# Performance work log

Hardware: AMD Instinct MI355X
Metric: run time of the kernel (lower is better)

The kernel has to match this reference:

```python
import jax, jax.numpy as jnp
import numpy as np
from jax import lax

PRE_NMS_THRESH = 0.05
PRE_NMS_TOP_N = 1000
FINAL_NMS_THRESH = 0.4  # hardcoded in forward(): boxlist_nms(..., 0.4)
MIN_SIZE = 0
STRIDE = 4.0
NEG = -1e9

N, C, H, W = 32, 1, 384, 384


def setup_inputs() -> dict:
    key = jax.random.key(0)
    k1, k2 = jax.random.split(key)
    box_cls = jax.random.uniform(k1, (N, C, H, W), dtype=jnp.float32)
    box_regression = jax.random.normal(k2, (N, 4, H, W), dtype=jnp.float32) * 20.0
    image_sizes = jnp.full((N, 2), H * int(STRIDE), dtype=jnp.int32)
    return {"box_cls": box_cls, "box_regression": box_regression, "image_sizes": image_sizes}


def decode_boxes(quad):
    # quad: [N, 4, H, W]; EAST geometry decode at stride 4 -> xyxy
    n, _, h, w = quad.shape
    x = (jnp.arange(w, dtype=quad.dtype) * STRIDE)[None, :]   # [1, W]
    y = (jnp.arange(h, dtype=quad.dtype) * STRIDE)[:, None]   # [H, 1]
    ymin = y - quad[:, 0]
    xmax = x + quad[:, 1]
    ymax = y + quad[:, 2]
    xmin = x - quad[:, 3]
    return jnp.stack([xmin, ymin, xmax, ymax], axis=1)  # [N, 4, H, W] (permute (3,0,1,2))


def iou_matrix(b):
    # b: [K, 4] xyxy
    x1, y1, x2, y2 = b[:, 0], b[:, 1], b[:, 2], b[:, 3]
    area = jnp.clip(x2 - x1, 0) * jnp.clip(y2 - y1, 0)
    ix1 = jnp.maximum(x1[:, None], x1[None, :])
    iy1 = jnp.maximum(y1[:, None], y1[None, :])
    ix2 = jnp.minimum(x2[:, None], x2[None, :])
    iy2 = jnp.minimum(y2[:, None], y2[None, :])
    inter = jnp.clip(ix2 - ix1, 0) * jnp.clip(iy2 - iy1, 0)
    union = area[:, None] + area[None, :] - inter
    return inter / jnp.maximum(union, 1e-9)


def greedy_nms(boxes, init_keep):
    # boxes: [K, 4] sorted by descending score; init_keep: [K] bool
    K = boxes.shape[0]
    iou = iou_matrix(boxes)
    idx = jnp.arange(K)

    def body(i, keep):
        suppress = (iou[i] > FINAL_NMS_THRESH) & (idx > i)
        return jnp.where(keep[i], keep & ~suppress, keep)

    return lax.fori_loop(0, K, body, init_keep)


def _forward(box_cls, box_regression):
    n, c, h, w = box_cls.shape
    boxes = decode_boxes(box_regression)                       # [N, 4, H, W]
    boxes = boxes.transpose(0, 2, 3, 1).reshape(n, h * w, 4)   # [N, HW, 4]
    scores = box_cls.transpose(0, 2, 3, 1).reshape(n, h * w)   # [N, HW] (C=1)

    # threshold + conditional top-k (padding with NEG emulates variable counts)
    masked = jnp.where(scores > PRE_NMS_THRESH, scores, NEG)
    scores_k, idx_k = lax.top_k(masked, PRE_NMS_TOP_N)         # [N, K], sorted desc
    boxes_k = jnp.take_along_axis(boxes, idx_k[..., None], axis=1)  # [N, K, 4]

    valid = scores_k > PRE_NMS_THRESH
    ws = boxes_k[..., 2] - boxes_k[..., 0]
    hs = boxes_k[..., 3] - boxes_k[..., 1]
    valid = valid & (ws >= MIN_SIZE) & (hs >= MIN_SIZE)        # remove_small_boxes

    keep = jax.vmap(greedy_nms)(boxes_k, valid)                # [N, K]
    out = jnp.concatenate([boxes_k, scores_k[..., None]], axis=-1)
    out = out * keep[..., None].astype(out.dtype)              # [N, K, 5]
    return out, keep


def reference(box_cls, box_regression, image_sizes):
    return _forward(box_cls, box_regression)
```

## Files before the change

### kernel.cpp

```cpp
#include <hip/hip_runtime.h>
#include <stdint.h>

#define NIMG 32
#define WID 384
#define HW 147456
#define TOPK 1000
#define KPAD 1024
#define NBINS 512
#define BIN_SCALEF 512.0f
#define SEGCAP 128
#define CANDCAP 2048
#define THRESH 0.05f
#define PREF_C 0.99f
#define NMS_T 0.4f
#define NBLK 18
#define FINEBINS 256

typedef unsigned long long u64;
typedef unsigned int u32;

#define PCNT_OFF 0
#define PCAND_OFF 4096
#define PBOX_OFF  593920

__device__ __forceinline__ float area_of(float x0, float y0, float x1, float y1) {
  float a = fmaxf(x1 - x0, 0.0f) * fmaxf(y1 - y0, 0.0f);
  asm volatile("" : "+v"(a));
  return a;
}

__device__ __forceinline__ bool iou_gt(float ax0, float ay0, float ax1, float ay1, float aa,
                                       float bx0, float by0, float bx1, float by1, float ba) {
  float ix1 = fmaxf(ax0, bx0);
  float iy1 = fmaxf(ay0, by0);
  float ix2 = fminf(ax1, bx1);
  float iy2 = fminf(ay1, by1);
  float iw = fmaxf(ix2 - ix1, 0.0f);
  float ih = fmaxf(iy2 - iy1, 0.0f);
  float inter = iw * ih;
  asm volatile("" : "+v"(inter));
  float uni = fmaxf(aa + ba - inter, 1e-9f);
  return (inter / uni) > NMS_T;
}

__device__ __forceinline__ u64 shflxor64(u64 v, int m) {
  int lo = __shfl_xor((int)(u32)v, m, 64);
  int hi = __shfl_xor((int)(u32)(v >> 32), m, 64);
  return ((u64)(u32)hi << 32) | (u32)lo;
}

__device__ __forceinline__ u64 make_key(float s, u32 idx) {
  u32 ord = __float_as_uint(s) | 0x80000000u;
  return ((u64)ord << 32) | (u32)(~idx);
}

__device__ __forceinline__ float score_of(u64 key) {
  return __uint_as_float((u32)(key >> 32) & 0x7FFFFFFFu);
}

__device__ __forceinline__ int bin_of(float s) {
  int b = (int)(s * BIN_SCALEF);
  return b < 0 ? 0 : (b > NBINS - 1 ? NBINS - 1 : b);
}

__device__ __forceinline__ int finebin(u64 key) {
  float s = score_of(key);
  int b = (int)((s - 0.99f) * 25600.0f);
  return b < 0 ? 0 : (b > FINEBINS - 1 ? FINEBINS - 1 : b);
}

__global__ __launch_bounds__(256) void scan_kernel(const float* __restrict__ cls,
                                                   const float* __restrict__ reg,
                                                   u32* __restrict__ pcnt,
                                                   u64* __restrict__ pcand,
                                                   float4* __restrict__ pbox) {
  __shared__ u64 lbuf[SEGCAP];
  __shared__ u32 lcnt;
  const int n = blockIdx.y;
  const int tid = threadIdx.x;
  const int lane = tid & 63;
  if (tid == 0) lcnt = 0;
  __syncthreads();

  const float4* src = (const float4*)(cls + (size_t)n * HW) + blockIdx.x * 2048;
  float4 A[8];
#pragma unroll
  for (int v = 0; v < 8; v++) A[v] = src[tid + v * 256];

  const u64 ltmask = (1ull << lane) - 1ull;
#pragma unroll
  for (int v = 0; v < 8; v++) {
    float ss[4] = {A[v].x, A[v].y, A[v].z, A[v].w};
#pragma unroll
    for (int c = 0; c < 4; c++) {
      float s = ss[c];
      bool pc = s > PREF_C;
      u64 m = __ballot(pc);
      if (m) {
        int ldr = __ffsll(m) - 1;
        u32 wb = 0;
        if (lane == ldr) wb = atomicAdd(&lcnt, (u32)__popcll(m));
        wb = (u32)__shfl((int)wb, ldr, 64);
        if (pc) {
          u32 pos = wb + (u32)__popcll(m & ltmask);
          if (pos < SEGCAP) lbuf[pos] = make_key(s, (u32)((blockIdx.x * 2048 + tid + v * 256) * 4 + c));
        }
      }
    }
  }
  __syncthreads();
  const int seg = n * NBLK + blockIdx.x;
  if (tid == 0) pcnt[seg] = (lcnt > SEGCAP) ? 0xFFFFFFFFu : lcnt;
  u32 c = lcnt < SEGCAP ? lcnt : (u32)SEGCAP;
  const float* rb = reg + (size_t)n * 4 * HW;
  u64* pk = pcand + (size_t)seg * SEGCAP;
  float4* pb = pbox + (size_t)seg * SEGCAP;
  for (u32 i = tid; i < c; i += 256) {
    u64 key = lbuf[i];
    u32 idx = ~(u32)(key & 0xFFFFFFFFull);
    int iy = (int)idx / WID;
    int ix = (int)idx - iy * WID;
    float xx = (float)ix * 4.0f;
    float yy = (float)iy * 4.0f;
    float r0 = rb[idx];
    float r1 = rb[HW + idx];
    float r2 = rb[2 * HW + idx];
    float r3 = rb[3 * HW + idx];
    float4 box;
    box.y = yy - r0; box.z = xx + r1; box.w = yy + r2; box.x = xx - r3;
    pk[i] = key;
    pb[i] = box;
  }
}

#define REGCHAIN(K, JSTART) do {                                            \
    const bool desc_ = ((tid & ((K) >> 1)) == 0);                           \
    for (int j_ = (JSTART); j_ >= 2; j_ >>= 1) {                            \
      int h_ = j_ >> 1;                                                     \
      bool low_ = (tid & h_) == 0;                                          \
      u64 p0_ = shflxor64(e0, h_), p1_ = shflxor64(e1, h_);                 \
      bool tm_ = (low_ == desc_);                                           \
      e0 = tm_ ? (e0 > p0_ ? e0 : p0_) : (e0 < p0_ ? e0 : p0_);             \
      e1 = tm_ ? (e1 > p1_ ? e1 : p1_) : (e1 < p1_ ? e1 : p1_);             \
    }                                                                       \
    { u64 lo_ = e0 < e1 ? e0 : e1, hi_ = e0 < e1 ? e1 : e0;                 \
      e0 = desc_ ? hi_ : lo_; e1 = desc_ ? lo_ : hi_; }                     \
  } while (0)

__global__ __launch_bounds__(1024) void fused_kernel(const float* __restrict__ cls,
                                                     const float* __restrict__ reg,
                                                     const u32* __restrict__ pcnt,
                                                     const u64* __restrict__ pcand,
                                                     const float4* __restrict__ pbox,
                                                     float* __restrict__ out) {
  __shared__ __align__(16) unsigned char smem[90112];
  u64*    CKEY   = (u64*)smem;
  float4* CBOX   = (float4*)(smem + 16384);
  u32*    BINNED = (u32*)(smem + 49152);
  u64*    RKEY   = (u64*)(smem + 57344);
  float4* RBOX   = (float4*)(smem + 65536);
  float* vx    = (float*)smem;
  float* vy    = (float*)(smem + 4096);
  float* vz    = (float*)(smem + 8192);
  float* vw    = (float*)(smem + 12288);
  float* varea = (float*)(smem + 16384);
  u64*   mlds  = (u64*)(smem + 20480);

  __shared__ u32 BINSTART[FINEBINS + 1];
  __shared__ u32 HIST[FINEBINS];
  __shared__ u32 scnt[NBLK];
  __shared__ u32 soff[NBLK];
  __shared__ u32 bs[NBINS];
  __shared__ u32 stmp[64];
  __shared__ int stbin;
  __shared__ u32 sflag, sfc;
  __shared__ int sC;
  __shared__ u32 wcnt[16], woff[16];
  __shared__ int pc[136], pk[136];
  __shared__ int sV, snch, snp;
  __shared__ u64 keepsh[16], srem[16];

  const int n = blockIdx.x;
  const int tid = threadIdx.x;
  const int lane = tid & 63;
  const int w = tid >> 6;
  const u64 ltmask = (1ull << lane) - 1ull;

  if (tid < NBLK) scnt[tid] = pcnt[n * NBLK + tid];
  RKEY[tid] = 0ull;
  if (tid < FINEBINS) HIST[tid] = 0;
  if (tid == 0) sfc = 0;
  __syncthreads();
  if (tid == 0) {
    u32 f = 0, off = 0;
    for (int s = 0; s < NBLK; s++) {
      u32 c = scnt[s];
      if (c == 0xFFFFFFFFu) { f = 1; c = 0; }
      soff[s] = off; off += c;
    }
    if (off < TOPK || off > CANDCAP) f = 1;
    sflag = f; sC = (int)off;
  }
  __syncthreads();

  u64 key; float4 b;

  if (sflag == 0) {
    const int C = sC;
    for (int seg = w; seg < NBLK; seg += 16) {
      u32 c = scnt[seg];
      u32 o = soff[seg];
      const u64* srck = pcand + (size_t)(n * NBLK + seg) * SEGCAP;
      const float4* srcb = pbox + (size_t)(n * NBLK + seg) * SEGCAP;
      for (u32 i = lane; i < c; i += 64) {
        CKEY[o + i] = srck[i];
        CBOX[o + i] = srcb[i];
      }
    }
    __syncthreads();
    for (int i = tid; i < C; i += 1024) atomicAdd(&HIST[finebin(CKEY[i])], 1u);
    __syncthreads();
    if (tid < 64) {
      u32 h0 = HIST[lane * 4 + 0], h1 = HIST[lane * 4 + 1];
      u32 h2 = HIST[lane * 4 + 2], h3 = HIST[lane * 4 + 3];
      u32 t = h0 + h1 + h2 + h3;
      u32 incl = t;
#pragma unroll
      for (int d = 1; d < 64; d <<= 1) {
        u32 v = (u32)__shfl_up((int)incl, d, 64);
        if (lane >= d) incl += v;
      }
      u32 base = incl - t;
      BINSTART[lane * 4 + 0] = base;
      BINSTART[lane * 4 + 1] = base + h0;
      BINSTART[lane * 4 + 2] = base + h0 + h1;
      BINSTART[lane * 4 + 3] = base + h0 + h1 + h2;
      if (lane == 63) BINSTART[FINEBINS] = incl;
      HIST[lane * 4 + 0] = 0; HIST[lane * 4 + 1] = 0;
      HIST[lane * 4 + 2] = 0; HIST[lane * 4 + 3] = 0;
    }
    __syncthreads();
    for (int i = tid; i < C; i += 1024) {
      int bb = finebin(CKEY[i]);
      u32 slot = atomicAdd(&HIST[bb], 1u);
      BINNED[BINSTART[bb] + slot] = (u32)i;
    }
    __syncthreads();
    for (int i = tid; i < C; i += 1024) {
      u64 k = CKEY[i];
      int bb = finebin(k);
      u32 s0 = BINSTART[bb], s1 = BINSTART[bb + 1];
      u32 g = 0;
      for (u32 j = s0; j < s1; j++) {
        u32 cj = BINNED[j];
        if (CKEY[cj] > k) g++;
      }
      u32 rank = (u32)C - s1 + g;
      if (rank < KPAD) { RKEY[rank] = k; RBOX[rank] = CBOX[i]; }
    }
    __syncthreads();
    key = RKEY[tid];
    b = (key != 0ull) ? RBOX[tid] : make_float4(0.f, 0.f, 0.f, 0.f);
  } else {
    for (int i = tid; i < NBINS; i += 1024) bs[i] = 0;
    CKEY[tid] = 0ull; CKEY[tid + 1024] = 0ull;
    __syncthreads();
    const float* ci = cls + (size_t)n * HW;
    for (int base = 0; base < HW; base += 1024) {
      float s = ci[base + tid];
      if (s > THRESH) atomicAdd(&bs[bin_of(s)], 1u);
    }
    __syncthreads();
    if (tid < 64) {
      u32 cs = 0;
#pragma unroll
      for (int k2 = 0; k2 < 8; k2++) cs += bs[lane * 8 + k2];
      u32 s = cs;
#pragma unroll
      for (int d = 1; d < 64; d <<= 1) {
        u32 v = (u32)__shfl_down((int)s, d, 64);
        if (lane + d < 64) s += v;
      }
      stmp[lane] = s;
      u64 mask = __ballot(s >= TOPK);
      if (lane == 0) {
        int t = 0;
        if (mask) {
          int L = 63 - __clzll(mask);
          u32 acc = (L < 63) ? stmp[L + 1] : 0;
          for (int bb = L * 8 + 7; bb >= L * 8; bb--) {
            acc += bs[bb];
            if (acc >= TOPK) { t = bb; break; }
          }
        }
        stbin = t;
      }
    }
    __syncthreads();
    const int t = stbin;
    for (int base = 0; base < HW; base += 1024) {
      int i = base + tid;
      float s = ci[i];
      bool p = (s > THRESH) && (bin_of(s) >= t);
      u64 m = __ballot(p);
      if (m) {
        int ldr = __ffsll(m) - 1;
        u32 wb = 0;
        if (lane == ldr) wb = atomicAdd(&sfc, (u32)__popcll(m));
        wb = (u32)__shfl((int)wb, ldr, 64);
        if (p) { u32 pos = wb + (u32)__popcll(m & ltmask); if (pos < CANDCAP) CKEY[pos] = make_key(s, (u32)i); }
      }
    }
    __syncthreads();
    {
      u64 e0 = CKEY[2 * tid], e1 = CKEY[2 * tid + 1];
      REGCHAIN(2, 1); REGCHAIN(4, 2); REGCHAIN(8, 4); REGCHAIN(16, 8);
      REGCHAIN(32, 16); REGCHAIN(64, 32); REGCHAIN(128, 64);
      for (int k = 256; k <= CANDCAP; k <<= 1) {
        CKEY[2 * tid] = e0; CKEY[2 * tid + 1] = e1;
        __syncthreads();
        for (int j = k >> 1; j >= 128; j >>= 1) {
          int i = ((tid & ~(j - 1)) << 1) | (tid & (j - 1));
          u64 a = CKEY[i], bb = CKEY[i + j];
          bool desc = ((i & k) == 0);
          if (desc ? (a < bb) : (a > bb)) { CKEY[i] = bb; CKEY[i + j] = a; }
          __syncthreads();
        }
        e0 = CKEY[2 * tid]; e1 = CKEY[2 * tid + 1];
        REGCHAIN(k, 64);
      }
      CKEY[2 * tid] = e0; CKEY[2 * tid + 1] = e1;
      __syncthreads();
    }
    key = CKEY[tid];
    b = make_float4(0.f, 0.f, 0.f, 0.f);
    if (key != 0ull && tid < TOPK) {
      u32 idx = ~(u32)(key & 0xFFFFFFFFull);
      int iy = (int)idx / WID;
      int ix = (int)idx - iy * WID;
      float xx = (float)ix * 4.0f;
      float yy = (float)iy * 4.0f;
      const float* rb = reg + (size_t)n * 4 * HW;
      float r0 = rb[idx];
      float r1 = rb[HW + idx];
      float r2 = rb[2 * HW + idx];
      float r3 = rb[3 * HW + idx];
      b.y = yy - r0; b.z = xx + r1; b.w = yy + r2; b.x = xx - r3;
    }
  }
  float s = score_of(key);
  __syncthreads();

  bool vb = (tid < TOPK) && (s > THRESH) && (b.z - b.x >= 0.0f) && (b.w - b.y >= 0.0f);
  vx[tid] = 0.0f; vy[tid] = 0.0f; vz[tid] = 0.0f; vw[tid] = 0.0f;
  varea[tid] = 0.0f;
  u64 vm = __ballot(vb);
  if (lane == 0) wcnt[w] = (u32)__popcll(vm);
  if (tid < 16) { srem[tid] = 0ull; keepsh[tid] = 0ull; }
  __syncthreads();
  if (tid == 0) {
    u32 off = 0;
    for (int i = 0; i < 16; i++) { woff[i] = off; off += wcnt[i]; }
    int V = (int)off;
    int nch = (V + 63) >> 6;
    sV = V; snch = nch; snp = nch * (nch + 1) / 2;
  }
  __syncthreads();
  const int V = sV, nch = snch, npairs = snp;

  int pos = -1;
  if (vb) {
    pos = (int)(woff[w] + (u32)__popcll(vm & ltmask));
    vx[pos] = b.x; vy[pos] = b.y; vz[pos] = b.z; vw[pos] = b.w;
    varea[pos] = area_of(b.x, b.y, b.z, b.w);
  }
  if (tid < npairs) {
    int p = tid, c = 0, base = 0;
    while (p >= base + (nch - c)) { base += nch - c; c++; }
    pc[tid] = c; pk[tid] = c + (p - base);
  }
  __syncthreads();

  for (int r = w; r < npairs * 64; r += 16) {
    int p = r >> 6, i = r & 63;
    int c = pc[p], k = pk[p];
    int ri = k * 64 + i;
    float rx0 = vx[ri], ry0 = vy[ri], rx1 = vz[ri], ry1 = vw[ri], ra = varea[ri];
    int ci = c * 64 + lane;
    float cx0 = vx[ci], cy0 = vy[ci], cx1 = vz[ci], cy1 = vw[ci], ca = varea[ci];
    bool pred = iou_gt(rx0, ry0, rx1, ry1, ra, cx0, cy0, cx1, cy1, ca);
    u64 m = __ballot(pred);
    if (lane == 0) mlds[r] = m;
  }
  __syncthreads();

  if (tid < 64) {
    for (int c = 0; c < nch; c++) {
      int pbase = c * nch - (c * (c - 1)) / 2 - c;
      u64 diag = mlds[(pbase + c) * 64 + lane];
      u64 ainit = (V >= (c + 1) * 64) ? ~0ull
                : ((V > c * 64) ? ((1ull << (V - c * 64)) - 1ull) : 0ull);
      u64 alive;
      {
        u64 a = ainit & ~srem[c];
        u32 alo2 = __builtin_amdgcn_readfirstlane((u32)a);
        u32 ahi2 = __builtin_amdgcn_readfirstlane((u32)(a >> 32));
        alive = ((u64)ahi2 << 32) | alo2;
      }
      u32 rlo = (u32)diag, rhi = (u32)(diag >> 32);
      u64 cur = alive;
      while (cur) {
        int i = __ffsll(cur) - 1;
        u32 rl = __builtin_amdgcn_readlane(rlo, i);
        u32 rh = __builtin_amdgcn_readlane(rhi, i);
        u64 rowi = ((u64)rh << 32) | rl;
        u64 lowmask = (i == 63) ? ~0ull : ((1ull << (i + 1)) - 1ull);
        rowi &= ~lowmask;
        alive &= ~rowi;
        cur &= ~rowi;
        cur &= cur - 1;
      }
      if (lane == 0) keepsh[c] = alive;
      const u64 K = alive;
      for (int k = c + 1; k < nch; k++) {
        bool sup = (mlds[(pbase + k) * 64 + lane] & K) != 0ull;
        u64 mres = __ballot(sup);
        if (lane == 0) srem[k] |= mres;
      }
    }
  }
  __syncthreads();

  u64 kb = (vb && pos >= 0) ? ((keepsh[pos >> 6] >> (pos & 63)) & 1ull) : 0ull;
  if (tid < TOPK) {
    float f = (float)kb;
    size_t ob = (size_t)n * (TOPK * 5) + (size_t)tid * 5;
    out[ob + 0] = kb ? b.x : 0.0f;
    out[ob + 1] = kb ? b.y : 0.0f;
    out[ob + 2] = kb ? b.z : 0.0f;
    out[ob + 3] = kb ? b.w : 0.0f;
    out[ob + 4] = kb ? s : 0.0f;
    out[(size_t)NIMG * TOPK * 5 + (size_t)n * TOPK + tid] = f;
  }
}

extern "C" void kernel_launch(void* const* d_in, const int* in_sizes, int n_in,
                              void* d_out, int out_size, void* d_ws, size_t ws_size,
                              hipStream_t stream) {
  const float* cls = (const float*)d_in[0];
  const float* reg = (const float*)d_in[1];
  float* out = (float*)d_out;

  uint8_t* ws = (uint8_t*)d_ws;
  u32* pcnt = (u32*)(ws + PCNT_OFF);
  u64* pcand = (u64*)(ws + PCAND_OFF);
  float4* pbox = (float4*)(ws + PBOX_OFF);

  scan_kernel<<<dim3(NBLK, NIMG), 256, 0, stream>>>(cls, reg, pcnt, pcand, pbox);
  fused_kernel<<<NIMG, 1024, 0, stream>>>(cls, reg, pcnt, pcand, pbox, out);
}
```

Measured before the change: 154.9 us.

## Merge scan and NMS kernels into one cooperative launch with grid sync

```diff
diff --git a/kernel.cpp b/kernel.cpp
--- a/kernel.cpp
+++ b/kernel.cpp
@@ -1,5 +1,8 @@
 #include <hip/hip_runtime.h>
+#include <hip/hip_cooperative_groups.h>
 #include <stdint.h>
+
+namespace cg = cooperative_groups;
 
 #define NIMG 32
 #define WID 384
@@ -8,12 +11,14 @@
 #define KPAD 1024
 #define NBINS 512
 #define BIN_SCALEF 512.0f
-#define SEGCAP 128
+#define NSEG 8
+#define SEGN (NIMG * NSEG)
+#define SEGV 4608
+#define SEGCAP 256
 #define CANDCAP 2048
 #define THRESH 0.05f
 #define PREF_C 0.99f
 #define NMS_T 0.4f
-#define NBLK 18
 #define FINEBINS 256
 
 typedef unsigned long long u64;
@@ -21,7 +26,7 @@
 
 #define PCNT_OFF 0
 #define PCAND_OFF 4096
-#define PBOX_OFF  593920
+#define PBOX_OFF 528384
 
 __device__ __forceinline__ float area_of(float x0, float y0, float x1, float y1) {
   float a = fmaxf(x1 - x0, 0.0f) * fmaxf(y1 - y0, 0.0f);
@@ -69,27 +74,27 @@
   return b < 0 ? 0 : (b > FINEBINS - 1 ? FINEBINS - 1 : b);
 }
 
-__global__ __launch_bounds__(256) void scan_kernel(const float* __restrict__ cls,
-                                                   const float* __restrict__ reg,
-                                                   u32* __restrict__ pcnt,
-                                                   u64* __restrict__ pcand,
-                                                   float4* __restrict__ pbox) {
+__device__ void phaseA(const float* __restrict__ cls, const float* __restrict__ reg,
+                       u32* __restrict__ pcnt, u64* __restrict__ pcand,
+                       float4* __restrict__ pbox, int bid) {
   __shared__ u64 lbuf[SEGCAP];
   __shared__ u32 lcnt;
-  const int n = blockIdx.y;
   const int tid = threadIdx.x;
   const int lane = tid & 63;
   if (tid == 0) lcnt = 0;
   __syncthreads();
 
-  const float4* src = (const float4*)(cls + (size_t)n * HW) + blockIdx.x * 2048;
-  float4 A[8];
+  const int n = bid >> 3;
+  const int sub = bid & 7;
+  const float4* src = (const float4*)(cls + (size_t)n * HW) + sub * SEGV;
+  float4 A[5];
 #pragma unroll
-  for (int v = 0; v < 8; v++) A[v] = src[tid + v * 256];
+  for (int v = 0; v < 4; v++) A[v] = src[tid + v * 1024];
+  A[4] = (tid < 512) ? src[tid + 4096] : make_float4(0.f, 0.f, 0.f, 0.f);
 
   const u64 ltmask = (1ull << lane) - 1ull;
 #pragma unroll
-  for (int v = 0; v < 8; v++) {
+  for (int v = 0; v < 5; v++) {
     float ss[4] = {A[v].x, A[v].y, A[v].z, A[v].w};
 #pragma unroll
     for (int c = 0; c < 4; c++) {
@@ -103,19 +108,18 @@
         wb = (u32)__shfl((int)wb, ldr, 64);
         if (pc) {
           u32 pos = wb + (u32)__popcll(m & ltmask);
-          if (pos < SEGCAP) lbuf[pos] = make_key(s, (u32)((blockIdx.x * 2048 + tid + v * 256) * 4 + c));
+          if (pos < SEGCAP) lbuf[pos] = make_key(s, (u32)((sub * SEGV + tid + v * 1024) * 4 + c));
         }
       }
     }
   }
   __syncthreads();
-  const int seg = n * NBLK + blockIdx.x;
-  if (tid == 0) pcnt[seg] = (lcnt > SEGCAP) ? 0xFFFFFFFFu : lcnt;
+  if (tid == 0) pcnt[bid] = (lcnt > SEGCAP) ? 0xFFFFFFFFu : lcnt;
   u32 c = lcnt < SEGCAP ? lcnt : (u32)SEGCAP;
   const float* rb = reg + (size_t)n * 4 * HW;
-  u64* pk = pcand + (size_t)seg * SEGCAP;
-  float4* pb = pbox + (size_t)seg * SEGCAP;
-  for (u32 i = tid; i < c; i += 256) {
+  u64* pk = pcand + (size_t)bid * SEGCAP;
+  float4* pb = pbox + (size_t)bid * SEGCAP;
+  for (u32 i = tid; i < c; i += 1024) {
     u64 key = lbuf[i];
     u32 idx = ~(u32)(key & 0xFFFFFFFFull);
     int iy = (int)idx / WID;
@@ -147,12 +151,9 @@
       e0 = desc_ ? hi_ : lo_; e1 = desc_ ? lo_ : hi_; }                     \
   } while (0)
 
-__global__ __launch_bounds__(1024) void fused_kernel(const float* __restrict__ cls,
-                                                     const float* __restrict__ reg,
-                                                     const u32* __restrict__ pcnt,
-                                                     const u64* __restrict__ pcand,
-                                                     const float4* __restrict__ pbox,
-                                                     float* __restrict__ out) {
+__device__ void phaseB(const float* __restrict__ cls, const float* __restrict__ reg,
+                       const u32* __restrict__ pcnt, const u64* __restrict__ pcand,
+                       const float4* __restrict__ pbox, float* __restrict__ out, int n) {
   __shared__ __align__(16) unsigned char smem[90112];
   u64*    CKEY   = (u64*)smem;
   float4* CBOX   = (float4*)(smem + 16384);
@@ -168,8 +169,8 @@
 
   __shared__ u32 BINSTART[FINEBINS + 1];
   __shared__ u32 HIST[FINEBINS];
-  __shared__ u32 scnt[NBLK];
-  __shared__ u32 soff[NBLK];
+  __shared__ u32 scnt[NSEG];
+  __shared__ u32 soff[NSEG];
   __shared__ u32 bs[NBINS];
   __shared__ u32 stmp[64];
   __shared__ int stbin;
@@ -180,20 +181,19 @@
   __shared__ int sV, snch, snp;
   __shared__ u64 keepsh[16], srem[16];
 
-  const int n = blockIdx.x;
   const int tid = threadIdx.x;
   const int lane = tid & 63;
   const int w = tid >> 6;
   const u64 ltmask = (1ull << lane) - 1ull;
 
-  if (tid < NBLK) scnt[tid] = pcnt[n * NBLK + tid];
+  if (tid < NSEG) scnt[tid] = pcnt[n * NSEG + tid];
   RKEY[tid] = 0ull;
   if (tid < FINEBINS) HIST[tid] = 0;
   if (tid == 0) sfc = 0;
   __syncthreads();
   if (tid == 0) {
     u32 f = 0, off = 0;
-    for (int s = 0; s < NBLK; s++) {
+    for (int s = 0; s < NSEG; s++) {
       u32 c = scnt[s];
       if (c == 0xFFFFFFFFu) { f = 1; c = 0; }
       soff[s] = off; off += c;
@@ -207,12 +207,12 @@
 
   if (sflag == 0) {
     const int C = sC;
-    for (int seg = w; seg < NBLK; seg += 16) {
-      u32 c = scnt[seg];
-      u32 o = soff[seg];
-      const u64* srck = pcand + (size_t)(n * NBLK + seg) * SEGCAP;
-      const float4* srcb = pbox + (size_t)(n * NBLK + seg) * SEGCAP;
-      for (u32 i = lane; i < c; i += 64) {
+    {
+      int s = tid >> 7;
+      u32 c = scnt[s], o = soff[s];
+      const u64* srck = pcand + (size_t)(n * NSEG + s) * SEGCAP;
+      const float4* srcb = pbox + (size_t)(n * NSEG + s) * SEGCAP;
+      for (u32 i = (u32)(tid & 127); i < c; i += 128) {
         CKEY[o + i] = srck[i];
         CBOX[o + i] = srcb[i];
       }
@@ -444,6 +444,34 @@
   }
 }
 
+__global__ __launch_bounds__(1024) void mega_kernel(const float* __restrict__ cls,
+                                                    const float* __restrict__ reg,
+                                                    u32* __restrict__ pcnt,
+                                                    u64* __restrict__ pcand,
+                                                    float4* __restrict__ pbox,
+                                                    float* __restrict__ out) {
+  phaseA(cls, reg, pcnt, pcand, pbox, blockIdx.x);
+  cg::this_grid().sync();
+  if (blockIdx.x < NIMG) phaseB(cls, reg, pcnt, pcand, pbox, out, blockIdx.x);
+}
+
+__global__ __launch_bounds__(1024) void phaseA_kernel(const float* __restrict__ cls,
+                                                      const float* __restrict__ reg,
+                                                      u32* __restrict__ pcnt,
+                                                      u64* __restrict__ pcand,
+                                                      float4* __restrict__ pbox) {
+  phaseA(cls, reg, pcnt, pcand, pbox, blockIdx.x);
+}
+
+__global__ __launch_bounds__(1024) void phaseB_kernel(const float* __restrict__ cls,
+                                                      const float* __restrict__ reg,
+                                                      const u32* __restrict__ pcnt,
+                                                      const u64* __restrict__ pcand,
+                                                      const float4* __restrict__ pbox,
+                                                      float* __restrict__ out) {
+  phaseB(cls, reg, pcnt, pcand, pbox, out, blockIdx.x);
+}
+
 extern "C" void kernel_launch(void* const* d_in, const int* in_sizes, int n_in,
                               void* d_out, int out_size, void* d_ws, size_t ws_size,
                               hipStream_t stream) {
@@ -456,6 +484,23 @@
   u64* pcand = (u64*)(ws + PCAND_OFF);
   float4* pbox = (float4*)(ws + PBOX_OFF);
 
-  scan_kernel<<<dim3(NBLK, NIMG), 256, 0, stream>>>(cls, reg, pcnt, pcand, pbox);
-  fused_kernel<<<NIMG, 1024, 0, stream>>>(cls, reg, pcnt, pcand, pbox, out);
-}
+  static int coop = -1;
+  if (coop < 0) {
+    int dev = 0, v = 0;
+    hipGetDevice(&dev);
+    hipDeviceGetAttribute(&v, hipDeviceAttributeCooperativeLaunch, dev);
+    coop = v ? 1 : 0;
+  }
+
+  bool done = false;
+  if (coop) {
+    void* args[] = {(void*)&cls, (void*)&reg, (void*)&pcnt, (void*)&pcand, (void*)&pbox, (void*)&out};
+    hipError_t e = hipLaunchCooperativeKernel((const void*)mega_kernel, dim3(SEGN), dim3(1024),
+                                              args, 0, stream);
+    done = (e == hipSuccess);
+  }
+  if (!done) {
+    phaseA_kernel<<<dim3(SEGN), 1024, 0, stream>>>(cls, reg, pcnt, pcand, pbox);
+    phaseB_kernel<<<dim3(NIMG), 1024, 0, stream>>>(cls, reg, pcnt, pcand, pbox, out);
+  }
+}
```

After: 209.1 us. +35.0%, slower.

## Merge scan and NMS kernels into one launch with atomic completion counters

Applied to the files above, without the earlier changes.

```diff
diff --git a/kernel.cpp b/kernel.cpp
--- a/kernel.cpp
+++ b/kernel.cpp
@@ -8,20 +8,25 @@
 #define KPAD 1024
 #define NBINS 512
 #define BIN_SCALEF 512.0f
-#define SEGCAP 128
+#define NSEG 6
+#define SEGN (NIMG * NSEG)
+#define SEGV4 6144
+#define SEGCAP 384
 #define CANDCAP 2048
 #define THRESH 0.05f
 #define PREF_C 0.99f
 #define NMS_T 0.4f
-#define NBLK 18
 #define FINEBINS 256
+#define GRID (SEGN + NIMG)
+#define SPIN_MAX 100000u
 
 typedef unsigned long long u64;
 typedef unsigned int u32;
 
-#define PCNT_OFF 0
+#define DONE_OFF 0
+#define PCNT_OFF 1024
 #define PCAND_OFF 4096
-#define PBOX_OFF  593920
+#define PBOX_OFF 593920
 
 __device__ __forceinline__ float area_of(float x0, float y0, float x1, float y1) {
   float a = fmaxf(x1 - x0, 0.0f) * fmaxf(y1 - y0, 0.0f);
@@ -67,70 +72,6 @@
   float s = score_of(key);
   int b = (int)((s - 0.99f) * 25600.0f);
   return b < 0 ? 0 : (b > FINEBINS - 1 ? FINEBINS - 1 : b);
-}
-
-__global__ __launch_bounds__(256) void scan_kernel(const float* __restrict__ cls,
-                                                   const float* __restrict__ reg,
-                                                   u32* __restrict__ pcnt,
-                                                   u64* __restrict__ pcand,
-                                                   float4* __restrict__ pbox) {
-  __shared__ u64 lbuf[SEGCAP];
-  __shared__ u32 lcnt;
-  const int n = blockIdx.y;
-  const int tid = threadIdx.x;
-  const int lane = tid & 63;
-  if (tid == 0) lcnt = 0;
-  __syncthreads();
-
-  const float4* src = (const float4*)(cls + (size_t)n * HW) + blockIdx.x * 2048;
-  float4 A[8];
-#pragma unroll
-  for (int v = 0; v < 8; v++) A[v] = src[tid + v * 256];
-
-  const u64 ltmask = (1ull << lane) - 1ull;
-#pragma unroll
-  for (int v = 0; v < 8; v++) {
-    float ss[4] = {A[v].x, A[v].y, A[v].z, A[v].w};
-#pragma unroll
-    for (int c = 0; c < 4; c++) {
-      float s = ss[c];
-      bool pc = s > PREF_C;
-      u64 m = __ballot(pc);
-      if (m) {
-        int ldr = __ffsll(m) - 1;
-        u32 wb = 0;
-        if (lane == ldr) wb = atomicAdd(&lcnt, (u32)__popcll(m));
-        wb = (u32)__shfl((int)wb, ldr, 64);
-        if (pc) {
-          u32 pos = wb + (u32)__popcll(m & ltmask);
-          if (pos < SEGCAP) lbuf[pos] = make_key(s, (u32)((blockIdx.x * 2048 + tid + v * 256) * 4 + c));
-        }
-      }
-    }
-  }
-  __syncthreads();
-  const int seg = n * NBLK + blockIdx.x;
-  if (tid == 0) pcnt[seg] = (lcnt > SEGCAP) ? 0xFFFFFFFFu : lcnt;
-  u32 c = lcnt < SEGCAP ? lcnt : (u32)SEGCAP;
-  const float* rb = reg + (size_t)n * 4 * HW;
-  u64* pk = pcand + (size_t)seg * SEGCAP;
-  float4* pb = pbox + (size_t)seg * SEGCAP;
-  for (u32 i = tid; i < c; i += 256) {
-    u64 key = lbuf[i];
-    u32 idx = ~(u32)(key & 0xFFFFFFFFull);
-    int iy = (int)idx / WID;
-    int ix = (int)idx - iy * WID;
-    float xx = (float)ix * 4.0f;
-    float yy = (float)iy * 4.0f;
-    float r0 = rb[idx];
-    float r1 = rb[HW + idx];
-    float r2 = rb[2 * HW + idx];
-    float r3 = rb[3 * HW + idx];
-    float4 box;
-    box.y = yy - r0; box.z = xx + r1; box.w = yy + r2; box.x = xx - r3;
-    pk[i] = key;
-    pb[i] = box;
-  }
 }
 
 #define REGCHAIN(K, JSTART) do {                                            \
@@ -147,12 +88,15 @@
       e0 = desc_ ? hi_ : lo_; e1 = desc_ ? lo_ : hi_; }                     \
   } while (0)
 
-__global__ __launch_bounds__(1024) void fused_kernel(const float* __restrict__ cls,
-                                                     const float* __restrict__ reg,
-                                                     const u32* __restrict__ pcnt,
-                                                     const u64* __restrict__ pcand,
-                                                     const float4* __restrict__ pbox,
-                                                     float* __restrict__ out) {
+__global__ __launch_bounds__(1024) void mega_kernel(const float* __restrict__ cls,
+                                                    const float* __restrict__ reg,
+                                                    u32* __restrict__ done,
+                                                    u32* __restrict__ pcnt,
+                                                    u64* __restrict__ pcand,
+                                                    float4* __restrict__ pbox,
+                                                    float* __restrict__ out) {
+  __shared__ u64 lbuf[SEGCAP];
+  __shared__ u32 lcnt;
   __shared__ __align__(16) unsigned char smem[90112];
   u64*    CKEY   = (u64*)smem;
   float4* CBOX   = (float4*)(smem + 16384);
@@ -168,8 +112,8 @@
 
   __shared__ u32 BINSTART[FINEBINS + 1];
   __shared__ u32 HIST[FINEBINS];
-  __shared__ u32 scnt[NBLK];
-  __shared__ u32 soff[NBLK];
+  __shared__ u32 scnt[NSEG];
+  __shared__ u32 soff[NSEG];
   __shared__ u32 bs[NBINS];
   __shared__ u32 stmp[64];
   __shared__ int stbin;
@@ -180,23 +124,96 @@
   __shared__ int sV, snch, snp;
   __shared__ u64 keepsh[16], srem[16];
 
-  const int n = blockIdx.x;
+  const int bid = blockIdx.x;
   const int tid = threadIdx.x;
   const int lane = tid & 63;
   const int w = tid >> 6;
   const u64 ltmask = (1ull << lane) - 1ull;
 
-  if (tid < NBLK) scnt[tid] = pcnt[n * NBLK + tid];
+  if (bid < SEGN) {
+    if (tid == 0) lcnt = 0;
+    __syncthreads();
+    const int n = bid / NSEG;
+    const int sub = bid - n * NSEG;
+    const float4* src = (const float4*)(cls + (size_t)n * HW) + sub * SEGV4;
+    float4 A[6];
+#pragma unroll
+    for (int v = 0; v < 6; v++) A[v] = src[tid + v * 1024];
+
+#pragma unroll
+    for (int v = 0; v < 6; v++) {
+      float ss[4] = {A[v].x, A[v].y, A[v].z, A[v].w};
+#pragma unroll
+      for (int c = 0; c < 4; c++) {
+        float s = ss[c];
+        bool pcd = s > PREF_C;
+        u64 m = __ballot(pcd);
+        if (m) {
+          int ldr = __ffsll(m) - 1;
+          u32 wb = 0;
+          if (lane == ldr) wb = atomicAdd(&lcnt, (u32)__popcll(m));
+          wb = (u32)__shfl((int)wb, ldr, 64);
+          if (pcd) {
+            u32 pos = wb + (u32)__popcll(m & ltmask);
+            if (pos < SEGCAP) lbuf[pos] = make_key(s, (u32)((sub * SEGV4 + tid + v * 1024) * 4 + c));
+          }
+        }
+      }
+    }
+    __syncthreads();
+    if (tid == 0) pcnt[bid] = (lcnt > SEGCAP) ? 0xFFFFFFFFu : lcnt;
+    u32 c = lcnt < SEGCAP ? lcnt : (u32)SEGCAP;
+    const float* rb = reg + (size_t)n * 4 * HW;
+    u64* pkk = pcand + (size_t)bid * SEGCAP;
+    float4* pbb = pbox + (size_t)bid * SEGCAP;
+    for (u32 i = tid; i < c; i += 1024) {
+      u64 key = lbuf[i];
+      u32 idx = ~(u32)(key & 0xFFFFFFFFull);
+      int iy = (int)idx / WID;
+      int ix = (int)idx - iy * WID;
+      float xx = (float)ix * 4.0f;
+      float yy = (float)iy * 4.0f;
+      float r0 = rb[idx];
+      float r1 = rb[HW + idx];
+      float r2 = rb[2 * HW + idx];
+      float r3 = rb[3 * HW + idx];
+      float4 box;
+      box.y = yy - r0; box.z = xx + r1; box.w = yy + r2; box.x = xx - r3;
+      pkk[i] = key;
+      pbb[i] = box;
+    }
+    __syncthreads();
+    if (tid == 0) {
+      __threadfence();
+      atomicAdd(&done[n], 1u);
+    }
+    return;
+  }
+
+  const int n = bid - SEGN;
+  u32 timeout = 0;
+  if (tid == 0) {
+    timeout = 1;
+    for (u32 it = 0; it < SPIN_MAX; ++it) {
+      if (atomicAdd(&done[n], 0u) >= (u32)NSEG) { timeout = 0; break; }
+      __builtin_amdgcn_s_sleep(32);
+    }
+  }
+  __syncthreads();
+  __threadfence();
+
+  if (tid < NSEG) scnt[tid] = pcnt[n * NSEG + tid];
   RKEY[tid] = 0ull;
   if (tid < FINEBINS) HIST[tid] = 0;
   if (tid == 0) sfc = 0;
   __syncthreads();
   if (tid == 0) {
-    u32 f = 0, off = 0;
-    for (int s = 0; s < NBLK; s++) {
-      u32 c = scnt[s];
-      if (c == 0xFFFFFFFFu) { f = 1; c = 0; }
-      soff[s] = off; off += c;
+    u32 f = timeout;
+    u32 off = 0;
+    for (int s = 0; s < NSEG; s++) {
+      u32 cc = scnt[s];
+      if (cc == 0xFFFFFFFFu) { f = 1; cc = 0; }
+      soff[s] = off; off += cc;
     }
     if (off < TOPK || off > CANDCAP) f = 1;
     sflag = f; sC = (int)off;
@@ -207,14 +224,13 @@
 
   if (sflag == 0) {
     const int C = sC;
-    for (int seg = w; seg < NBLK; seg += 16) {
-      u32 c = scnt[seg];
-      u32 o = soff[seg];
-      const u64* srck = pcand + (size_t)(n * NBLK + seg) * SEGCAP;
-      const float4* srcb = pbox + (size_t)(n * NBLK + seg) * SEGCAP;
-      for (u32 i = lane; i < c; i += 64) {
-        CKEY[o + i] = srck[i];
-        CBOX[o + i] = srcb[i];
+    for (int slot = tid; slot < NSEG * SEGCAP; slot += 1024) {
+      int s = slot / SEGCAP;
+      int i = slot - s * SEGCAP;
+      if ((u32)i < scnt[s]) {
+        u32 o = soff[s] + (u32)i;
+        CKEY[o] = pcand[(size_t)(n * NSEG + s) * SEGCAP + i];
+        CBOX[o] = pbox[(size_t)(n * NSEG + s) * SEGCAP + i];
       }
     }
     __syncthreads();
@@ -452,10 +468,11 @@
   float* out = (float*)d_out;
 
   uint8_t* ws = (uint8_t*)d_ws;
+  u32* done = (u32*)(ws + DONE_OFF);
   u32* pcnt = (u32*)(ws + PCNT_OFF);
   u64* pcand = (u64*)(ws + PCAND_OFF);
   float4* pbox = (float4*)(ws + PBOX_OFF);
 
-  scan_kernel<<<dim3(NBLK, NIMG), 256, 0, stream>>>(cls, reg, pcnt, pcand, pbox);
-  fused_kernel<<<NIMG, 1024, 0, stream>>>(cls, reg, pcnt, pcand, pbox, out);
-}
+  hipMemsetAsync(done, 0, NIMG * sizeof(u32), stream);
+  mega_kernel<<<dim3(GRID), 1024, 0, stream>>>(cls, reg, done, pcnt, pcand, pbox, out);
+}
```

New measurement: 171.0 us. 10.4% more time.

## Compact candidates per image via global atomics and prefetch them into registers

Applied to the files above, without the earlier changes.

```diff
diff --git a/kernel.cpp b/kernel.cpp
--- a/kernel.cpp
+++ b/kernel.cpp
@@ -19,9 +19,9 @@
 typedef unsigned long long u64;
 typedef unsigned int u32;
 
-#define PCNT_OFF 0
+#define PIMG_OFF 0
 #define PCAND_OFF 4096
-#define PBOX_OFF  593920
+#define PBOX_OFF 528384
 
 __device__ __forceinline__ float area_of(float x0, float y0, float x1, float y1) {
   float a = fmaxf(x1 - x0, 0.0f) * fmaxf(y1 - y0, 0.0f);
@@ -71,11 +71,11 @@
 
 __global__ __launch_bounds__(256) void scan_kernel(const float* __restrict__ cls,
                                                    const float* __restrict__ reg,
-                                                   u32* __restrict__ pcnt,
+                                                   u32* __restrict__ pimgcnt,
                                                    u64* __restrict__ pcand,
                                                    float4* __restrict__ pbox) {
   __shared__ u64 lbuf[SEGCAP];
-  __shared__ u32 lcnt;
+  __shared__ u32 lcnt, sbase;
   const int n = blockIdx.y;
   const int tid = threadIdx.x;
   const int lane = tid & 63;
@@ -109,27 +109,35 @@
     }
   }
   __syncthreads();
-  const int seg = n * NBLK + blockIdx.x;
-  if (tid == 0) pcnt[seg] = (lcnt > SEGCAP) ? 0xFFFFFFFFu : lcnt;
-  u32 c = lcnt < SEGCAP ? lcnt : (u32)SEGCAP;
+  const u32 total = lcnt;
+  const u32 c = total < SEGCAP ? total : (u32)SEGCAP;
+  if (tid == 0) {
+    u32 add = (total > SEGCAP) ? (c + 0x100000u) : c;
+    sbase = atomicAdd(&pimgcnt[n], add);
+  }
+  __syncthreads();
+  const u32 base = sbase;
   const float* rb = reg + (size_t)n * 4 * HW;
-  u64* pk = pcand + (size_t)seg * SEGCAP;
-  float4* pb = pbox + (size_t)seg * SEGCAP;
+  u64* pk = pcand + (size_t)n * CANDCAP;
+  float4* pb = pbox + (size_t)n * CANDCAP;
   for (u32 i = tid; i < c; i += 256) {
-    u64 key = lbuf[i];
-    u32 idx = ~(u32)(key & 0xFFFFFFFFull);
-    int iy = (int)idx / WID;
-    int ix = (int)idx - iy * WID;
-    float xx = (float)ix * 4.0f;
-    float yy = (float)iy * 4.0f;
-    float r0 = rb[idx];
-    float r1 = rb[HW + idx];
-    float r2 = rb[2 * HW + idx];
-    float r3 = rb[3 * HW + idx];
-    float4 box;
-    box.y = yy - r0; box.z = xx + r1; box.w = yy + r2; box.x = xx - r3;
-    pk[i] = key;
-    pb[i] = box;
+    u32 slot = base + i;
+    if (slot < CANDCAP) {
+      u64 key = lbuf[i];
+      u32 idx = ~(u32)(key & 0xFFFFFFFFull);
+      int iy = (int)idx / WID;
+      int ix = (int)idx - iy * WID;
+      float xx = (float)ix * 4.0f;
+      float yy = (float)iy * 4.0f;
+      float r0 = rb[idx];
+      float r1 = rb[HW + idx];
+      float r2 = rb[2 * HW + idx];
+      float r3 = rb[3 * HW + idx];
+      float4 box;
+      box.y = yy - r0; box.z = xx + r1; box.w = yy + r2; box.x = xx - r3;
+      pk[slot] = key;
+      pb[slot] = box;
+    }
   }
 }
 
@@ -149,7 +157,7 @@
 
 __global__ __launch_bounds__(1024) void fused_kernel(const float* __restrict__ cls,
                                                      const float* __restrict__ reg,
-                                                     const u32* __restrict__ pcnt,
+                                                     const u32* __restrict__ pimgcnt,
                                                      const u64* __restrict__ pcand,
                                                      const float4* __restrict__ pbox,
                                                      float* __restrict__ out) {
@@ -168,8 +176,6 @@
 
   __shared__ u32 BINSTART[FINEBINS + 1];
   __shared__ u32 HIST[FINEBINS];
-  __shared__ u32 scnt[NBLK];
-  __shared__ u32 soff[NBLK];
   __shared__ u32 bs[NBINS];
   __shared__ u32 stmp[64];
   __shared__ int stbin;
@@ -186,20 +192,20 @@
   const int w = tid >> 6;
   const u64 ltmask = (1ull << lane) - 1ull;
 
-  if (tid < NBLK) scnt[tid] = pcnt[n * NBLK + tid];
+  const u64* gk = pcand + (size_t)n * CANDCAP;
+  const float4* gb = pbox + (size_t)n * CANDCAP;
+  u64 k0 = gk[tid];
+  u64 k1 = gk[tid + 1024];
+  float4 b0 = gb[tid];
+  float4 b1 = gb[tid + 1024];
+
   RKEY[tid] = 0ull;
   if (tid < FINEBINS) HIST[tid] = 0;
-  if (tid == 0) sfc = 0;
-  __syncthreads();
   if (tid == 0) {
-    u32 f = 0, off = 0;
-    for (int s = 0; s < NBLK; s++) {
-      u32 c = scnt[s];
-      if (c == 0xFFFFFFFFu) { f = 1; c = 0; }
-      soff[s] = off; off += c;
-    }
-    if (off < TOPK || off > CANDCAP) f = 1;
-    sflag = f; sC = (int)off;
+    u32 C = pimgcnt[n];
+    sC = (int)C;
+    sflag = (C < TOPK || C > CANDCAP) ? 1u : 0u;
+    sfc = 0;
   }
   __syncthreads();
 
@@ -207,18 +213,8 @@
 
   if (sflag == 0) {
     const int C = sC;
-    for (int seg = w; seg < NBLK; seg += 16) {
-      u32 c = scnt[seg];
-      u32 o = soff[seg];
-      const u64* srck = pcand + (size_t)(n * NBLK + seg) * SEGCAP;
-      const float4* srcb = pbox + (size_t)(n * NBLK + seg) * SEGCAP;
-      for (u32 i = lane; i < c; i += 64) {
-        CKEY[o + i] = srck[i];
-        CBOX[o + i] = srcb[i];
-      }
-    }
-    __syncthreads();
-    for (int i = tid; i < C; i += 1024) atomicAdd(&HIST[finebin(CKEY[i])], 1u);
+    if (tid < C)        { CKEY[tid] = k0;        CBOX[tid] = b0;        atomicAdd(&HIST[finebin(k0)], 1u); }
+    if (tid + 1024 < C) { CKEY[tid + 1024] = k1; CBOX[tid + 1024] = b1; atomicAdd(&HIST[finebin(k1)], 1u); }
     __syncthreads();
     if (tid < 64) {
       u32 h0 = HIST[lane * 4 + 0], h1 = HIST[lane * 4 + 1];
@@ -240,23 +236,34 @@
       HIST[lane * 4 + 2] = 0; HIST[lane * 4 + 3] = 0;
     }
     __syncthreads();
-    for (int i = tid; i < C; i += 1024) {
-      int bb = finebin(CKEY[i]);
+    if (tid < C) {
+      int bb = finebin(k0);
       u32 slot = atomicAdd(&HIST[bb], 1u);
-      BINNED[BINSTART[bb] + slot] = (u32)i;
-    }
-    __syncthreads();
-    for (int i = tid; i < C; i += 1024) {
-      u64 k = CKEY[i];
+      BINNED[BINSTART[bb] + slot] = (u32)tid;
+    }
+    if (tid + 1024 < C) {
+      int bb = finebin(k1);
+      u32 slot = atomicAdd(&HIST[bb], 1u);
+      BINNED[BINSTART[bb] + slot] = (u32)(tid + 1024);
+    }
+    __syncthreads();
+    if (tid < C) {
+      u64 k = k0;
       int bb = finebin(k);
       u32 s0 = BINSTART[bb], s1 = BINSTART[bb + 1];
       u32 g = 0;
-      for (u32 j = s0; j < s1; j++) {
-        u32 cj = BINNED[j];
-        if (CKEY[cj] > k) g++;
-      }
+      for (u32 j = s0; j < s1; j++) { if (CKEY[BINNED[j]] > k) g++; }
       u32 rank = (u32)C - s1 + g;
-      if (rank < KPAD) { RKEY[rank] = k; RBOX[rank] = CBOX[i]; }
+      if (rank < KPAD) { RKEY[rank] = k; RBOX[rank] = b0; }
+    }
+    if (tid + 1024 < C) {
+      u64 k = k1;
+      int bb = finebin(k);
+      u32 s0 = BINSTART[bb], s1 = BINSTART[bb + 1];
+      u32 g = 0;
+      for (u32 j = s0; j < s1; j++) { if (CKEY[BINNED[j]] > k) g++; }
+      u32 rank = (u32)C - s1 + g;
+      if (rank < KPAD) { RKEY[rank] = k; RBOX[rank] = b1; }
     }
     __syncthreads();
     key = RKEY[tid];
@@ -358,12 +365,20 @@
   if (lane == 0) wcnt[w] = (u32)__popcll(vm);
   if (tid < 16) { srem[tid] = 0ull; keepsh[tid] = 0ull; }
   __syncthreads();
-  if (tid == 0) {
-    u32 off = 0;
-    for (int i = 0; i < 16; i++) { woff[i] = off; off += wcnt[i]; }
-    int V = (int)off;
-    int nch = (V + 63) >> 6;
-    sV = V; snch = nch; snp = nch * (nch + 1) / 2;
+  if (tid < 64) {
+    u32 v = (lane < 16) ? wcnt[lane] : 0u;
+    u32 incl = v;
+#pragma unroll
+    for (int d = 1; d < 16; d <<= 1) {
+      u32 t = (u32)__shfl_up((int)incl, d, 64);
+      if (lane >= d) incl += t;
+    }
+    if (lane < 16) woff[lane] = incl - v;
+    if (lane == 15) {
+      int V = (int)incl;
+      int nch = (V + 63) >> 6;
+      sV = V; snch = nch; snp = nch * (nch + 1) / 2;
+    }
   }
   __syncthreads();
   const int V = sV, nch = snch, npairs = snp;
@@ -381,16 +396,23 @@
   }
   __syncthreads();
 
-  for (int r = w; r < npairs * 64; r += 16) {
-    int p = r >> 6, i = r & 63;
-    int c = pc[p], k = pk[p];
-    int ri = k * 64 + i;
-    float rx0 = vx[ri], ry0 = vy[ri], rx1 = vz[ri], ry1 = vw[ri], ra = varea[ri];
-    int ci = c * 64 + lane;
-    float cx0 = vx[ci], cy0 = vy[ci], cx1 = vz[ci], cy1 = vw[ci], ca = varea[ci];
-    bool pred = iou_gt(rx0, ry0, rx1, ry1, ra, cx0, cy0, cx1, cy1, ca);
-    u64 m = __ballot(pred);
-    if (lane == 0) mlds[r] = m;
+  {
+    int prevc = -1;
+    float cx0 = 0.f, cy0 = 0.f, cx1 = 0.f, cy1 = 0.f, ca = 0.f;
+    for (int r = w; r < npairs * 64; r += 16) {
+      int p = r >> 6, i = r & 63;
+      int c = pc[p], k = pk[p];
+      if (c != prevc) {
+        int ci = c * 64 + lane;
+        cx0 = vx[ci]; cy0 = vy[ci]; cx1 = vz[ci]; cy1 = vw[ci]; ca = varea[ci];
+        prevc = c;
+      }
+      int ri = k * 64 + i;
+      float rx0 = vx[ri], ry0 = vy[ri], rx1 = vz[ri], ry1 = vw[ri], ra = varea[ri];
+      bool pred = iou_gt(rx0, ry0, rx1, ry1, ra, cx0, cy0, cx1, cy1, ca);
+      u64 m = __ballot(pred);
+      if (lane == 0) mlds[r] = m;
+    }
   }
   __syncthreads();
 
@@ -452,10 +474,11 @@
   float* out = (float*)d_out;
 
   uint8_t* ws = (uint8_t*)d_ws;
-  u32* pcnt = (u32*)(ws + PCNT_OFF);
+  u32* pimgcnt = (u32*)(ws + PIMG_OFF);
   u64* pcand = (u64*)(ws + PCAND_OFF);
   float4* pbox = (float4*)(ws + PBOX_OFF);
 
-  scan_kernel<<<dim3(NBLK, NIMG), 256, 0, stream>>>(cls, reg, pcnt, pcand, pbox);
-  fused_kernel<<<NIMG, 1024, 0, stream>>>(cls, reg, pcnt, pcand, pbox, out);
-}
+  hipMemsetAsync(pimgcnt, 0, NIMG * sizeof(u32), stream);
+  scan_kernel<<<dim3(NBLK, NIMG), 256, 0, stream>>>(cls, reg, pimgcnt, pcand, pbox);
+  fused_kernel<<<NIMG, 1024, 0, stream>>>(cls, reg, pimgcnt, pcand, pbox, out);
+}
```

After: 157.1 us. No clear change (+1.4%).
